# Kernel optimization log

Hardware: AMD Instinct MI355X
Metric: run time of the kernel (lower is better)

Reference implementation:

```python
import jax, jax.numpy as jnp
import numpy as np

TOKENS = 512
IN_F = 8192
OUT_F = 8192
RANK = 64
NNZ = 8192
QMAX = 127.0  # int8 symmetric


def setup_inputs() -> dict:
    key = jax.random.key(0)
    ks = jax.random.split(key, 12)
    x = jax.random.normal(ks[0], (TOKENS, IN_F), dtype=jnp.float32)
    quantized_weight = jax.random.randint(ks[1], (OUT_F, IN_F), -128, 128, dtype=jnp.int32)
    weight_scale = jax.random.uniform(ks[2], (OUT_F,), minval=0.005, maxval=0.02, dtype=jnp.float32)
    smooth_scales = jax.random.uniform(ks[3], (IN_F,), minval=0.5, maxval=2.0, dtype=jnp.float32)
    act_scale = jnp.array([0.05], dtype=jnp.float32)
    outlier_rows = jax.random.randint(ks[4], (NNZ,), 0, OUT_F, dtype=jnp.int32)
    outlier_cols = jax.random.randint(ks[5], (NNZ,), 0, IN_F, dtype=jnp.int32)
    outlier_vals = jax.random.normal(ks[6], (NNZ,), dtype=jnp.float32) * 0.1
    svd_U = jax.random.normal(ks[7], (OUT_F, RANK), dtype=jnp.float32) * 0.02
    svd_S = jax.random.uniform(ks[8], (RANK,), minval=0.1, maxval=1.0, dtype=jnp.float32)
    svd_V = jax.random.normal(ks[9], (IN_F, RANK), dtype=jnp.float32) * 0.02
    bias = jax.random.normal(ks[10], (OUT_F,), dtype=jnp.float32) * 0.01
    return {"x": x, "quantized_weight": quantized_weight, "weight_scale": weight_scale,
            "smooth_scales": smooth_scales, "act_scale": act_scale,
            "outlier_rows": outlier_rows, "outlier_cols": outlier_cols,
            "outlier_vals": outlier_vals, "svd_U": svd_U, "svd_S": svd_S,
            "svd_V": svd_V, "bias": bias}


def reference(x, quantized_weight, weight_scale, smooth_scales, act_scale,
              outlier_rows, outlier_cols, outlier_vals, svd_U, svd_S, svd_V, bias):
    # SmoothQuant: migrate activation outliers into the weight scales
    x_s = x / smooth_scales  # [T, in]
    # per-tensor symmetric int8 activation fake-quant
    a = act_scale[0]
    x_q = jnp.clip(jnp.round(x_s / a), -QMAX - 1.0, QMAX)
    x_dq = x_q * a  # [T, in]
    # dequantize weight: per-output-channel scale, plus sparse outlier correction
    W = quantized_weight.astype(jnp.float32) * weight_scale[:, None]  # [out, in]
    W = W.at[outlier_rows, outlier_cols].add(outlier_vals)
    # dense quantized matmul
    y = x_dq @ W.T  # [T, out]
    # low-rank SVD residual: x @ (U S V^T)^T = ((x @ V) * S) @ U^T
    y = y + ((x_dq @ svd_V) * svd_S) @ svd_U.T
    return y + bias
```

## Files before the change

### kernel.cpp

```cpp
#include <hip/hip_runtime.h>
#include <hip/hip_bf16.h>

#define TOKENS 512
#define IN_F 8192
#define OUT_F 8192
#define RANK 64
#define NNZ 8192

#define KSPLIT 4
#define KRANGE (IN_F / KSPLIT)
#define BM 512
#define BN 64
#define BK 64
#define NT (KRANGE / BK)

typedef __attribute__((ext_vector_type(8))) short short8;
typedef __attribute__((ext_vector_type(4))) float f32x4;
typedef __attribute__((ext_vector_type(4))) int int4v;

__device__ __forceinline__ unsigned short f2bf(float f) {
  unsigned int u = __builtin_bit_cast(unsigned int, f);
  u += 0x7FFFu + ((u >> 16) & 1u);
  return (unsigned short)(u >> 16);
}
__device__ __forceinline__ float bf2f(unsigned short b) {
  unsigned int u = ((unsigned int)b) << 16;
  return __builtin_bit_cast(float, u);
}

__device__ __forceinline__ void gload_lds16(const void* g, void* l) {
  __builtin_amdgcn_global_load_lds(
      (const __attribute__((address_space(1))) unsigned int*)(g),
      (__attribute__((address_space(3))) unsigned int*)(l), 16, 0, 0);
}

#define WAIT_VM(n) asm volatile("s_waitcnt vmcnt(" #n ")" ::: "memory")
#define WAIT_LGKM0 asm volatile("s_waitcnt lgkmcnt(0)" ::: "memory")

__global__ __launch_bounds__(256) void k_quant(const float* __restrict__ x,
                                               const float* __restrict__ smooth,
                                               const float* __restrict__ act,
                                               unsigned short* __restrict__ Abf,
                                               unsigned char* __restrict__ Aq) {
  int idx = blockIdx.x * 256 + threadIdx.x;
  int base = idx * 4;
  int col = base & (IN_F - 1);
  float a = act[0];
  float4 xx = *(const float4*)(x + base);
  float4 ss = *(const float4*)(smooth + col);
  float q0 = fminf(fmaxf(rintf((xx.x / ss.x) / a), -128.f), 127.f);
  float q1 = fminf(fmaxf(rintf((xx.y / ss.y) / a), -128.f), 127.f);
  float q2 = fminf(fmaxf(rintf((xx.z / ss.z) / a), -128.f), 127.f);
  float q3 = fminf(fmaxf(rintf((xx.w / ss.w) / a), -128.f), 127.f);
  ushort4 o;
  o.x = f2bf(q0); o.y = f2bf(q1); o.z = f2bf(q2); o.w = f2bf(q3);
  *(ushort4*)(Abf + base) = o;
  int i0 = (int)q0, i1 = (int)q1, i2 = (int)q2, i3 = (int)q3;
  unsigned int p = (i0 & 0xFF) | ((i1 & 0xFF) << 8) | ((i2 & 0xFF) << 16) |
                   ((unsigned)(i3 & 0xFF) << 24);
  *(unsigned int*)(Aq + base) = p;
}

__global__ __launch_bounds__(256) void k_lr1(const unsigned short* __restrict__ Abf,
                                             const float* __restrict__ V,
                                             const float* __restrict__ S,
                                             const float* __restrict__ act,
                                             float* __restrict__ t) {
  int bid = blockIdx.x;
  int mb = (bid & 3) * 128;
  int kb0 = (bid >> 2) * 512;
  int tid = threadIdx.x, w = tid >> 6, l = tid & 63;
  int lr = l & 15, lg = l >> 4;
  f32x4 acc[2][4] = {};
  for (int ks = 0; ks < 16; ++ks) {
    int kb = kb0 + ks * 32;
    short8 af[2];
#pragma unroll
    for (int fi = 0; fi < 2; ++fi) {
      int row = mb + w * 32 + fi * 16 + lr;
      af[fi] = *(const short8*)(Abf + (size_t)row * IN_F + kb + lg * 8);
    }
    short8 bfr[4];
#pragma unroll
    for (int fj = 0; fj < 4; ++fj) {
      int rk = fj * 16 + lr;
      short8 bv;
#pragma unroll
      for (int j = 0; j < 8; ++j)
        bv[j] = (short)f2bf(V[(size_t)(kb + lg * 8 + j) * RANK + rk]);
      bfr[fj] = bv;
    }
#pragma unroll
    for (int fi = 0; fi < 2; ++fi)
#pragma unroll
      for (int fj = 0; fj < 4; ++fj)
        acc[fi][fj] = __builtin_amdgcn_mfma_f32_16x16x32_bf16(af[fi], bfr[fj], acc[fi][fj], 0, 0, 0);
  }
  float a = act[0];
#pragma unroll
  for (int fi = 0; fi < 2; ++fi)
#pragma unroll
    for (int fj = 0; fj < 4; ++fj) {
      int rk = fj * 16 + lr;
      float sc = a * S[rk];
#pragma unroll
      for (int r = 0; r < 4; ++r) {
        int tok = mb + w * 32 + fi * 16 + lg * 4 + r;
        atomicAdd(t + tok * RANK + rk, acc[fi][fj][r] * sc);
      }
    }
}

__global__ __launch_bounds__(256) void k_lr2(const float* __restrict__ t,
                                             const float* __restrict__ U,
                                             const float* __restrict__ bias,
                                             float* __restrict__ out) {
  int bid = blockIdx.x;
  int mb = (bid & 3) * 128;
  int nb = (bid >> 2) * 128;
  int tid = threadIdx.x, w = tid >> 6, l = tid & 63;
  int lr = l & 15, lg = l >> 4;
  int wm = w >> 1, wn = w & 1;
  f32x4 acc[4][4] = {};
#pragma unroll
  for (int kk = 0; kk < 2; ++kk) {
    short8 af[4], bfr[4];
#pragma unroll
    for (int fi = 0; fi < 4; ++fi) {
      int row = mb + wm * 64 + fi * 16 + lr;
      const float4* tp = (const float4*)(t + (size_t)row * RANK + kk * 32 + lg * 8);
      float4 t0 = tp[0], t1 = tp[1];
      af[fi][0] = f2bf(t0.x); af[fi][1] = f2bf(t0.y);
      af[fi][2] = f2bf(t0.z); af[fi][3] = f2bf(t0.w);
      af[fi][4] = f2bf(t1.x); af[fi][5] = f2bf(t1.y);
      af[fi][6] = f2bf(t1.z); af[fi][7] = f2bf(t1.w);
    }
#pragma unroll
    for (int fj = 0; fj < 4; ++fj) {
      int row = nb + wn * 64 + fj * 16 + lr;
      const float4* up = (const float4*)(U + (size_t)row * RANK + kk * 32 + lg * 8);
      float4 u0 = up[0], u1 = up[1];
      bfr[fj][0] = f2bf(u0.x); bfr[fj][1] = f2bf(u0.y);
      bfr[fj][2] = f2bf(u0.z); bfr[fj][3] = f2bf(u0.w);
      bfr[fj][4] = f2bf(u1.x); bfr[fj][5] = f2bf(u1.y);
      bfr[fj][6] = f2bf(u1.z); bfr[fj][7] = f2bf(u1.w);
    }
#pragma unroll
    for (int fi = 0; fi < 4; ++fi)
#pragma unroll
      for (int fj = 0; fj < 4; ++fj)
        acc[fi][fj] = __builtin_amdgcn_mfma_f32_16x16x32_bf16(af[fi], bfr[fj], acc[fi][fj], 0, 0, 0);
  }
#pragma unroll
  for (int fj = 0; fj < 4; ++fj) {
    int o = nb + wn * 64 + fj * 16 + lr;
    float b = bias[o];
#pragma unroll
    for (int fi = 0; fi < 4; ++fi)
#pragma unroll
      for (int r = 0; r < 4; ++r) {
        int tok = mb + wm * 64 + fi * 16 + lg * 4 + r;
        out[(size_t)tok * OUT_F + o] = b + acc[fi][fj][r];
      }
  }
}

__global__ __launch_bounds__(256) void k_outlier_merge(
    const unsigned short* __restrict__ Abf, const int* __restrict__ rows,
    const int* __restrict__ cols, const float* __restrict__ vals,
    const float* __restrict__ act, const float* __restrict__ wscale,
    const int* __restrict__ part, float* __restrict__ out) {
  __shared__ float accr[OUT_F];
  int tk = blockIdx.x;
  for (int i = threadIdx.x; i < OUT_F; i += 256) accr[i] = 0.f;
  __syncthreads();
  float a = act[0];
  for (int i = threadIdx.x; i < NNZ; i += 256) {
    int r = rows[i], c = cols[i];
    float v = vals[i];
    float xq = bf2f(Abf[(size_t)tk * IN_F + c]);
    atomicAdd(accr + r, a * xq * v);
  }
  __syncthreads();
  float* orow = out + (size_t)tk * OUT_F;
  const int* p0 = part + (size_t)tk * OUT_F;
  const int* p1 = p0 + (size_t)TOKENS * OUT_F;
  const int* p2 = p1 + (size_t)TOKENS * OUT_F;
  const int* p3 = p2 + (size_t)TOKENS * OUT_F;
  for (int i = threadIdx.x * 4; i < OUT_F; i += 1024) {
    int4v s0 = *(const int4v*)(p0 + i);
    int4v s1 = *(const int4v*)(p1 + i);
    int4v s2 = *(const int4v*)(p2 + i);
    int4v s3 = *(const int4v*)(p3 + i);
    float4 ws = *(const float4*)(wscale + i);
    float4 ov = *(const float4*)(orow + i);
    ov.x += accr[i + 0] + (float)(s0[0] + s1[0] + s2[0] + s3[0]) * a * ws.x;
    ov.y += accr[i + 1] + (float)(s0[1] + s1[1] + s2[1] + s3[1]) * a * ws.y;
    ov.z += accr[i + 2] + (float)(s0[2] + s1[2] + s2[2] + s3[2]) * a * ws.z;
    ov.w += accr[i + 3] + (float)(s0[3] + s1[3] + s2[3] + s3[3]) * a * ws.w;
    *(float4*)(orow + i) = ov;
  }
}

__global__ __launch_bounds__(512, 4) void k_gemm(const unsigned char* __restrict__ Aq,
                                                 const int* __restrict__ W,
                                                 int* __restrict__ part) {
  __shared__ __align__(16) unsigned char As[2][BM * BK];
  __shared__ __align__(16) unsigned char Bs[2][BN * BK];

  int d = blockIdx.x;
  int wg = (d & 7) * 64 + (d >> 3);
  int ks = wg >> 7;
  int nb = wg & 127;
  int kb0 = ks * KRANGE;

  int tid = threadIdx.x, w = tid >> 6, l = tid & 63;
  int lr = l & 15, lg = l >> 4;
  int wm = w >> 1, wn = w & 1;

  int4v acc[8][2] = {};
  int4v wa[2], wb[2];

  const int rB = tid >> 3;
  const int kcB = (tid & 7) * 8;

  auto LOAD_W = [&](int4v (&wr)[2], int kb) {
    const int* wp = W + (size_t)(nb * BN + rB) * IN_F + kb + kcB;
    wr[0] = *(const int4v*)wp;
    wr[1] = *(const int4v*)(wp + 4);
  };
  auto STAGE_A = [&](int buf, int kb) {
#pragma unroll
    for (int i = 0; i < 4; ++i) {
      int ubase = i * 512 + w * 64;
      int ell = ubase + l;
      int r = ell >> 2, up = ell & 3;
      int u = up ^ ((r >> 1) & 3);
      gload_lds16(Aq + (size_t)r * IN_F + kb + u * 16, &As[buf][(size_t)ubase * 16]);
    }
  };
  auto WRITE_B = [&](int buf, const int4v (&wr)[2]) {
    unsigned int w0 = 0, w1 = 0;
#pragma unroll
    for (int j = 0; j < 4; ++j) w0 |= ((unsigned)(wr[0][j] & 0xFF)) << (8 * j);
#pragma unroll
    for (int j = 0; j < 4; ++j) w1 |= ((unsigned)(wr[1][j] & 0xFF)) << (8 * j);
    int u = kcB >> 4, sub = (kcB >> 3) & 1;
    int us = u ^ ((rB >> 1) & 3);
    uint2 val; val.x = w0; val.y = w1;
    *(uint2*)(&Bs[buf][(size_t)rB * BK + us * 16 + sub * 8]) = val;
  };
  auto LDFA = [&](int buf, int row) -> int4v {
    int u = lg ^ ((row >> 1) & 3);
    return *(const int4v*)(&As[buf][(size_t)row * BK + u * 16]);
  };
  auto LDFB = [&](int buf, int row) -> int4v {
    int u = lg ^ ((row >> 1) & 3);
    return *(const int4v*)(&Bs[buf][(size_t)row * BK + u * 16]);
  };
  auto COMPUTE = [&](int buf) {
    __builtin_amdgcn_s_setprio(1);
    int4v b0 = LDFB(buf, wn * 32 + lr);
    int4v b1 = LDFB(buf, wn * 32 + 16 + lr);
#pragma unroll
    for (int fi = 0; fi < 8; ++fi) {
      int4v af = LDFA(buf, wm * 128 + fi * 16 + lr);
      acc[fi][0] = __builtin_amdgcn_mfma_i32_16x16x64_i8(af, b0, acc[fi][0], 0, 0, 0);
      acc[fi][1] = __builtin_amdgcn_mfma_i32_16x16x64_i8(af, b1, acc[fi][1], 0, 0, 0);
    }
    __builtin_amdgcn_s_setprio(0);
  };

  LOAD_W(wa, kb0);
  STAGE_A(0, kb0);
  WAIT_VM(4);
  WRITE_B(0, wa);
  LOAD_W(wa, kb0 + BK);
  WAIT_VM(2);
  WAIT_LGKM0;
  __builtin_amdgcn_s_barrier();

#define ITER(kt, CUR, wcur, wnxt)                                   \
  {                                                                 \
    STAGE_A(CUR ^ 1, kb0 + (((kt) + 1) & (NT - 1)) * BK);           \
    LOAD_W(wnxt, kb0 + (((kt) + 2) & (NT - 1)) * BK);               \
    COMPUTE(CUR);                                                   \
    WAIT_VM(6);                                                     \
    WRITE_B(CUR ^ 1, wcur);                                         \
    WAIT_VM(2);                                                     \
    WAIT_LGKM0;                                                     \
    __builtin_amdgcn_s_barrier();                                   \
  }

  for (int kt = 0; kt < NT; kt += 2) {
    ITER(kt, 0, wa, wb);
    ITER(kt + 1, 1, wb, wa);
  }
#undef ITER

  int* pp = part + (size_t)ks * TOKENS * OUT_F;
#pragma unroll
  for (int fj = 0; fj < 2; ++fj) {
    int o = nb * BN + wn * 32 + fj * 16 + lr;
#pragma unroll
    for (int fi = 0; fi < 8; ++fi)
#pragma unroll
      for (int rr = 0; rr < 4; ++rr) {
        int tok = wm * 128 + fi * 16 + lg * 4 + rr;
        pp[(size_t)tok * OUT_F + o] = acc[fi][fj][rr];
      }
  }
}

extern "C" void kernel_launch(void* const* d_in, const int* in_sizes, int n_in,
                              void* d_out, int out_size, void* d_ws, size_t ws_size,
                              hipStream_t stream) {
  const float* x = (const float*)d_in[0];
  const int* W = (const int*)d_in[1];
  const float* wscale = (const float*)d_in[2];
  const float* smooth = (const float*)d_in[3];
  const float* act = (const float*)d_in[4];
  const int* orow = (const int*)d_in[5];
  const int* ocol = (const int*)d_in[6];
  const float* oval = (const float*)d_in[7];
  const float* U = (const float*)d_in[8];
  const float* S = (const float*)d_in[9];
  const float* V = (const float*)d_in[10];
  const float* bias = (const float*)d_in[11];
  float* out = (float*)d_out;

  unsigned short* Abf = (unsigned short*)d_ws;
  unsigned char* Aq = (unsigned char*)d_ws + (size_t)TOKENS * IN_F * 2;
  float* t = (float*)((char*)d_ws + (size_t)TOKENS * IN_F * 3);
  int* part = (int*)((char*)d_ws + (size_t)TOKENS * IN_F * 3 + (size_t)TOKENS * RANK * 4);

  hipMemsetAsync(t, 0, TOKENS * RANK * sizeof(float), stream);
  k_quant<<<(TOKENS * IN_F / 4) / 256, 256, 0, stream>>>(x, smooth, act, Abf, Aq);
  k_gemm<<<512, 512, 0, stream>>>(Aq, W, part);
  k_lr1<<<64, 256, 0, stream>>>(Abf, V, S, act, t);
  k_lr2<<<256, 256, 0, stream>>>(t, U, bias, out);
  k_outlier_merge<<<TOKENS, 256, 0, stream>>>(Abf, orow, ocol, oval, act,
                                              wscale, part, out);
}
```

Measured before the change: 191.1 us.

## Widen GEMM N-tile to 128 with 1024-thread blocks and triple-buffered LDS

The int8 GEMM now uses BN=128 tiles and 1024-thread workgroups, so half as many blocks launch (256) and each warp holds a 4x4 fragment grid instead of 8x2. LDS staging moves from double to triple buffering, with A prefetched two k-steps ahead, plus sched_barrier fences around the workgroup barriers. The aim is to halve redundant A-tile traffic per output column, raise MFMA work per LDS fragment load, and hide global-load latency better. The cost is more LDS per block and fewer blocks per CU, and 256 blocks may leave some of the device's compute units without work.

```diff
diff --git a/kernel.cpp b/kernel.cpp
--- a/kernel.cpp
+++ b/kernel.cpp
@@ -10,7 +10,7 @@
 #define KSPLIT 4
 #define KRANGE (IN_F / KSPLIT)
 #define BM 512
-#define BN 64
+#define BN 128
 #define BK 64
 #define NT (KRANGE / BK)
 
@@ -36,6 +36,7 @@
 
 #define WAIT_VM(n) asm volatile("s_waitcnt vmcnt(" #n ")" ::: "memory")
 #define WAIT_LGKM0 asm volatile("s_waitcnt lgkmcnt(0)" ::: "memory")
+#define SCHED0 __builtin_amdgcn_sched_barrier(0)
 
 __global__ __launch_bounds__(256) void k_quant(const float* __restrict__ x,
                                                const float* __restrict__ smooth,
@@ -202,53 +203,55 @@
   }
 }
 
-__global__ __launch_bounds__(512, 4) void k_gemm(const unsigned char* __restrict__ Aq,
-                                                 const int* __restrict__ W,
-                                                 int* __restrict__ part) {
-  __shared__ __align__(16) unsigned char As[2][BM * BK];
-  __shared__ __align__(16) unsigned char Bs[2][BN * BK];
+__global__ __launch_bounds__(1024, 4) void k_gemm(const unsigned char* __restrict__ Aq,
+                                                  const int* __restrict__ W,
+                                                  int* __restrict__ part) {
+  __shared__ __align__(16) unsigned char As[3][BM * BK];
+  __shared__ __align__(16) unsigned char Bs[3][BN * BK];
 
   int d = blockIdx.x;
-  int wg = (d & 7) * 64 + (d >> 3);
-  int ks = wg >> 7;
-  int nb = wg & 127;
+  int wg = (d & 7) * 32 + (d >> 3);
+  int ks = wg >> 6;
+  int nb = wg & 63;
   int kb0 = ks * KRANGE;
 
   int tid = threadIdx.x, w = tid >> 6, l = tid & 63;
   int lr = l & 15, lg = l >> 4;
   int wm = w >> 1, wn = w & 1;
 
-  int4v acc[8][2] = {};
+  int4v acc[4][4] = {};
   int4v wa[2], wb[2];
 
-  const int rB = tid >> 3;
-  const int kcB = (tid & 7) * 8;
-
-  auto LOAD_W = [&](int4v (&wr)[2], int kb) {
-    const int* wp = W + (size_t)(nb * BN + rB) * IN_F + kb + kcB;
+  const int rW = tid >> 3;
+  const int kcW = (tid & 7) * 8;
+  const int uW = (kcW >> 4) ^ ((rW >> 1) & 3);
+  const int offW = kcW & 15;
+
+  auto LOAD_W = [&](int4v (&wr)[2], int kt) {
+    const int* wp = W + (size_t)(nb * BN + rW) * IN_F + kb0 +
+                    (kt & (NT - 1)) * BK + kcW;
     wr[0] = *(const int4v*)wp;
     wr[1] = *(const int4v*)(wp + 4);
   };
-  auto STAGE_A = [&](int buf, int kb) {
-#pragma unroll
-    for (int i = 0; i < 4; ++i) {
-      int ubase = i * 512 + w * 64;
-      int ell = ubase + l;
-      int r = ell >> 2, up = ell & 3;
+  auto STAGE_A = [&](int buf, int kt) {
+    int kb = kb0 + (kt & (NT - 1)) * BK;
+#pragma unroll
+    for (int i = 0; i < 2; ++i) {
+      int lidx = i * 1024 + w * 64;
+      int U = lidx + l;
+      int r = U >> 2, up = U & 3;
       int u = up ^ ((r >> 1) & 3);
-      gload_lds16(Aq + (size_t)r * IN_F + kb + u * 16, &As[buf][(size_t)ubase * 16]);
-    }
-  };
-  auto WRITE_B = [&](int buf, const int4v (&wr)[2]) {
+      gload_lds16(Aq + (size_t)r * IN_F + kb + u * 16, &As[buf][(size_t)lidx * 16]);
+    }
+  };
+  auto DSWRITE_B = [&](int buf, const int4v (&wr)[2]) {
     unsigned int w0 = 0, w1 = 0;
 #pragma unroll
     for (int j = 0; j < 4; ++j) w0 |= ((unsigned)(wr[0][j] & 0xFF)) << (8 * j);
 #pragma unroll
     for (int j = 0; j < 4; ++j) w1 |= ((unsigned)(wr[1][j] & 0xFF)) << (8 * j);
-    int u = kcB >> 4, sub = (kcB >> 3) & 1;
-    int us = u ^ ((rB >> 1) & 3);
     uint2 val; val.x = w0; val.y = w1;
-    *(uint2*)(&Bs[buf][(size_t)rB * BK + us * 16 + sub * 8]) = val;
+    *(uint2*)(&Bs[buf][(size_t)rW * BK + uW * 16 + offW]) = val;
   };
   auto LDFA = [&](int buf, int row) -> int4v {
     int u = lg ^ ((row >> 1) & 3);
@@ -259,54 +262,67 @@
     return *(const int4v*)(&Bs[buf][(size_t)row * BK + u * 16]);
   };
   auto COMPUTE = [&](int buf) {
+    int4v b0 = LDFB(buf, wn * 64 + 0 * 16 + lr);
+    int4v b1 = LDFB(buf, wn * 64 + 1 * 16 + lr);
+    int4v b2 = LDFB(buf, wn * 64 + 2 * 16 + lr);
+    int4v b3 = LDFB(buf, wn * 64 + 3 * 16 + lr);
     __builtin_amdgcn_s_setprio(1);
-    int4v b0 = LDFB(buf, wn * 32 + lr);
-    int4v b1 = LDFB(buf, wn * 32 + 16 + lr);
-#pragma unroll
-    for (int fi = 0; fi < 8; ++fi) {
-      int4v af = LDFA(buf, wm * 128 + fi * 16 + lr);
+#pragma unroll
+    for (int fi = 0; fi < 4; ++fi) {
+      int4v af = LDFA(buf, wm * 64 + fi * 16 + lr);
       acc[fi][0] = __builtin_amdgcn_mfma_i32_16x16x64_i8(af, b0, acc[fi][0], 0, 0, 0);
       acc[fi][1] = __builtin_amdgcn_mfma_i32_16x16x64_i8(af, b1, acc[fi][1], 0, 0, 0);
+      acc[fi][2] = __builtin_amdgcn_mfma_i32_16x16x64_i8(af, b2, acc[fi][2], 0, 0, 0);
+      acc[fi][3] = __builtin_amdgcn_mfma_i32_16x16x64_i8(af, b3, acc[fi][3], 0, 0, 0);
     }
     __builtin_amdgcn_s_setprio(0);
   };
 
-  LOAD_W(wa, kb0);
-  STAGE_A(0, kb0);
+  STAGE_A(0, 0);
+  LOAD_W(wa, 0);
+  STAGE_A(1, 1);
+  LOAD_W(wb, 1);
   WAIT_VM(4);
-  WRITE_B(0, wa);
-  LOAD_W(wa, kb0 + BK);
-  WAIT_VM(2);
+  DSWRITE_B(0, wa);
   WAIT_LGKM0;
+  SCHED0;
   __builtin_amdgcn_s_barrier();
-
-#define ITER(kt, CUR, wcur, wnxt)                                   \
-  {                                                                 \
-    STAGE_A(CUR ^ 1, kb0 + (((kt) + 1) & (NT - 1)) * BK);           \
-    LOAD_W(wnxt, kb0 + (((kt) + 2) & (NT - 1)) * BK);               \
-    COMPUTE(CUR);                                                   \
-    WAIT_VM(6);                                                     \
-    WRITE_B(CUR ^ 1, wcur);                                         \
-    WAIT_VM(2);                                                     \
-    WAIT_LGKM0;                                                     \
-    __builtin_amdgcn_s_barrier();                                   \
-  }
-
+  SCHED0;
+
+  int c = 0;
   for (int kt = 0; kt < NT; kt += 2) {
-    ITER(kt, 0, wa, wb);
-    ITER(kt + 1, 1, wb, wa);
-  }
-#undef ITER
+    int c1 = c + 1 == 3 ? 0 : c + 1;
+    int c2 = c1 + 1 == 3 ? 0 : c1 + 1;
+    STAGE_A(c2, kt + 2);
+    LOAD_W(wa, kt + 2);
+    COMPUTE(c);
+    WAIT_VM(4);
+    DSWRITE_B(c1, wb);
+    WAIT_LGKM0;
+    SCHED0;
+    __builtin_amdgcn_s_barrier();
+    SCHED0;
+    STAGE_A(c, kt + 3);
+    LOAD_W(wb, kt + 3);
+    COMPUTE(c1);
+    WAIT_VM(4);
+    DSWRITE_B(c2, wa);
+    WAIT_LGKM0;
+    SCHED0;
+    __builtin_amdgcn_s_barrier();
+    SCHED0;
+    c = c2;
+  }
 
   int* pp = part + (size_t)ks * TOKENS * OUT_F;
 #pragma unroll
-  for (int fj = 0; fj < 2; ++fj) {
-    int o = nb * BN + wn * 32 + fj * 16 + lr;
-#pragma unroll
-    for (int fi = 0; fi < 8; ++fi)
+  for (int fj = 0; fj < 4; ++fj) {
+    int o = nb * BN + wn * 64 + fj * 16 + lr;
+#pragma unroll
+    for (int fi = 0; fi < 4; ++fi)
 #pragma unroll
       for (int rr = 0; rr < 4; ++rr) {
-        int tok = wm * 128 + fi * 16 + lg * 4 + rr;
+        int tok = wm * 64 + fi * 16 + lg * 4 + rr;
         pp[(size_t)tok * OUT_F + o] = acc[fi][fj][rr];
       }
   }
@@ -332,11 +348,12 @@
   unsigned short* Abf = (unsigned short*)d_ws;
   unsigned char* Aq = (unsigned char*)d_ws + (size_t)TOKENS * IN_F * 2;
   float* t = (float*)((char*)d_ws + (size_t)TOKENS * IN_F * 3);
-  int* part = (int*)((char*)d_ws + (size_t)TOKENS * IN_F * 3 + (size_t)TOKENS * RANK * 4);
+  int* part = (int*)((char*)d_ws + (size_t)TOKENS * IN_F * 3 +
+                     (size_t)TOKENS * RANK * 4);
 
   hipMemsetAsync(t, 0, TOKENS * RANK * sizeof(float), stream);
   k_quant<<<(TOKENS * IN_F / 4) / 256, 256, 0, stream>>>(x, smooth, act, Abf, Aq);
-  k_gemm<<<512, 512, 0, stream>>>(Aq, W, part);
+  k_gemm<<<256, 1024, 0, stream>>>(Aq, W, part);
   k_lr1<<<64, 256, 0, stream>>>(Abf, V, S, act, t);
   k_lr2<<<256, 256, 0, stream>>>(t, U, bias, out);
   k_outlier_merge<<<TOKENS, 256, 0, stream>>>(Abf, orow, ocol, oval, act,
```

New measurement: 185.6 us, median of 2. -2.9%, faster.

## Replace low-rank atomics with split partials and tighten GEMM pipeline scheduling

Applied to the files above, without the earlier changes.

The first low-rank kernel now writes per-K-split partial results to separate buffers instead of using atomicAdd, and the second low-rank kernel sums the 16 partials when it loads them. This removes the memset and the atomic contention. The int8 GEMM loop moves the B LDS write after a single vmcnt wait, sets priority only after the B fragment loads, and adds sched_barriers around the workgroup barrier to control instruction ordering. In exchange, workspace use grows and lr2 reads 16 times more data for t.

```diff
diff --git a/kernel.cpp b/kernel.cpp
--- a/kernel.cpp
+++ b/kernel.cpp
@@ -13,6 +13,7 @@
 #define BN 64
 #define BK 64
 #define NT (KRANGE / BK)
+#define LRSPLIT 16
 
 typedef __attribute__((ext_vector_type(8))) short short8;
 typedef __attribute__((ext_vector_type(4))) float f32x4;
@@ -36,6 +37,7 @@
 
 #define WAIT_VM(n) asm volatile("s_waitcnt vmcnt(" #n ")" ::: "memory")
 #define WAIT_LGKM0 asm volatile("s_waitcnt lgkmcnt(0)" ::: "memory")
+#define SCHED0 __builtin_amdgcn_sched_barrier(0)
 
 __global__ __launch_bounds__(256) void k_quant(const float* __restrict__ x,
                                                const float* __restrict__ smooth,
@@ -68,7 +70,8 @@
                                              float* __restrict__ t) {
   int bid = blockIdx.x;
   int mb = (bid & 3) * 128;
-  int kb0 = (bid >> 2) * 512;
+  int ksp = bid >> 2;
+  int kb0 = ksp * 512;
   int tid = threadIdx.x, w = tid >> 6, l = tid & 63;
   int lr = l & 15, lg = l >> 4;
   f32x4 acc[2][4] = {};
@@ -97,6 +100,7 @@
         acc[fi][fj] = __builtin_amdgcn_mfma_f32_16x16x32_bf16(af[fi], bfr[fj], acc[fi][fj], 0, 0, 0);
   }
   float a = act[0];
+  float* tk = t + (size_t)ksp * TOKENS * RANK;
 #pragma unroll
   for (int fi = 0; fi < 2; ++fi)
 #pragma unroll
@@ -106,7 +110,7 @@
 #pragma unroll
       for (int r = 0; r < 4; ++r) {
         int tok = mb + w * 32 + fi * 16 + lg * 4 + r;
-        atomicAdd(t + tok * RANK + rk, acc[fi][fj][r] * sc);
+        tk[(size_t)tok * RANK + rk] = acc[fi][fj][r] * sc;
       }
     }
 }
@@ -128,8 +132,14 @@
 #pragma unroll
     for (int fi = 0; fi < 4; ++fi) {
       int row = mb + wm * 64 + fi * 16 + lr;
-      const float4* tp = (const float4*)(t + (size_t)row * RANK + kk * 32 + lg * 8);
-      float4 t0 = tp[0], t1 = tp[1];
+      size_t off = (size_t)row * RANK + kk * 32 + lg * 8;
+      float4 t0 = {0, 0, 0, 0}, t1 = {0, 0, 0, 0};
+      for (int s = 0; s < LRSPLIT; ++s) {
+        const float4* tp = (const float4*)(t + (size_t)s * TOKENS * RANK + off);
+        float4 u0 = tp[0], u1 = tp[1];
+        t0.x += u0.x; t0.y += u0.y; t0.z += u0.z; t0.w += u0.w;
+        t1.x += u1.x; t1.y += u1.y; t1.z += u1.z; t1.w += u1.w;
+      }
       af[fi][0] = f2bf(t0.x); af[fi][1] = f2bf(t0.y);
       af[fi][2] = f2bf(t0.z); af[fi][3] = f2bf(t0.w);
       af[fi][4] = f2bf(t1.x); af[fi][5] = f2bf(t1.y);
@@ -221,34 +231,36 @@
   int4v acc[8][2] = {};
   int4v wa[2], wb[2];
 
-  const int rB = tid >> 3;
-  const int kcB = (tid & 7) * 8;
-
-  auto LOAD_W = [&](int4v (&wr)[2], int kb) {
-    const int* wp = W + (size_t)(nb * BN + rB) * IN_F + kb + kcB;
+  const int rW = tid >> 3;
+  const int kcW = (tid & 7) * 8;
+  const int uW = (kcW >> 4) ^ ((rW >> 1) & 3);
+  const int offW = kcW & 15;
+
+  auto LOAD_W = [&](int4v (&wr)[2], int kt) {
+    const int* wp = W + (size_t)(nb * BN + rW) * IN_F + kb0 +
+                    (kt & (NT - 1)) * BK + kcW;
     wr[0] = *(const int4v*)wp;
     wr[1] = *(const int4v*)(wp + 4);
   };
-  auto STAGE_A = [&](int buf, int kb) {
+  auto STAGE_A = [&](int buf, int kt) {
+    int kb = kb0 + (kt & (NT - 1)) * BK;
 #pragma unroll
     for (int i = 0; i < 4; ++i) {
-      int ubase = i * 512 + w * 64;
-      int ell = ubase + l;
-      int r = ell >> 2, up = ell & 3;
+      int lidx = i * 512 + w * 64;
+      int U = lidx + l;
+      int r = U >> 2, up = U & 3;
       int u = up ^ ((r >> 1) & 3);
-      gload_lds16(Aq + (size_t)r * IN_F + kb + u * 16, &As[buf][(size_t)ubase * 16]);
-    }
-  };
-  auto WRITE_B = [&](int buf, const int4v (&wr)[2]) {
+      gload_lds16(Aq + (size_t)r * IN_F + kb + u * 16, &As[buf][(size_t)lidx * 16]);
+    }
+  };
+  auto DSWRITE_B = [&](int buf, const int4v (&wr)[2]) {
     unsigned int w0 = 0, w1 = 0;
 #pragma unroll
     for (int j = 0; j < 4; ++j) w0 |= ((unsigned)(wr[0][j] & 0xFF)) << (8 * j);
 #pragma unroll
     for (int j = 0; j < 4; ++j) w1 |= ((unsigned)(wr[1][j] & 0xFF)) << (8 * j);
-    int u = kcB >> 4, sub = (kcB >> 3) & 1;
-    int us = u ^ ((rB >> 1) & 3);
     uint2 val; val.x = w0; val.y = w1;
-    *(uint2*)(&Bs[buf][(size_t)rB * BK + us * 16 + sub * 8]) = val;
+    *(uint2*)(&Bs[buf][(size_t)rW * BK + uW * 16 + offW]) = val;
   };
   auto LDFA = [&](int buf, int row) -> int4v {
     int u = lg ^ ((row >> 1) & 3);
@@ -259,9 +271,9 @@
     return *(const int4v*)(&Bs[buf][(size_t)row * BK + u * 16]);
   };
   auto COMPUTE = [&](int buf) {
-    __builtin_amdgcn_s_setprio(1);
     int4v b0 = LDFB(buf, wn * 32 + lr);
     int4v b1 = LDFB(buf, wn * 32 + 16 + lr);
+    __builtin_amdgcn_s_setprio(1);
 #pragma unroll
     for (int fi = 0; fi < 8; ++fi) {
       int4v af = LDFA(buf, wm * 128 + fi * 16 + lr);
@@ -271,25 +283,28 @@
     __builtin_amdgcn_s_setprio(0);
   };
 
-  LOAD_W(wa, kb0);
-  STAGE_A(0, kb0);
+  LOAD_W(wa, 0);
+  STAGE_A(0, 0);
   WAIT_VM(4);
-  WRITE_B(0, wa);
-  LOAD_W(wa, kb0 + BK);
+  DSWRITE_B(0, wa);
+  LOAD_W(wa, 1);
   WAIT_VM(2);
   WAIT_LGKM0;
+  SCHED0;
   __builtin_amdgcn_s_barrier();
+  SCHED0;
 
 #define ITER(kt, CUR, wcur, wnxt)                                   \
   {                                                                 \
-    STAGE_A(CUR ^ 1, kb0 + (((kt) + 1) & (NT - 1)) * BK);           \
-    LOAD_W(wnxt, kb0 + (((kt) + 2) & (NT - 1)) * BK);               \
+    STAGE_A(CUR ^ 1, (kt) + 1);                                     \
+    LOAD_W(wnxt, (kt) + 2);                                         \
     COMPUTE(CUR);                                                   \
-    WAIT_VM(6);                                                     \
-    WRITE_B(CUR ^ 1, wcur);                                         \
     WAIT_VM(2);                                                     \
+    DSWRITE_B(CUR ^ 1, wcur);                                       \
     WAIT_LGKM0;                                                     \
+    SCHED0;                                                         \
     __builtin_amdgcn_s_barrier();                                   \
+    SCHED0;                                                         \
   }
 
   for (int kt = 0; kt < NT; kt += 2) {
@@ -332,9 +347,9 @@
   unsigned short* Abf = (unsigned short*)d_ws;
   unsigned char* Aq = (unsigned char*)d_ws + (size_t)TOKENS * IN_F * 2;
   float* t = (float*)((char*)d_ws + (size_t)TOKENS * IN_F * 3);
-  int* part = (int*)((char*)d_ws + (size_t)TOKENS * IN_F * 3 + (size_t)TOKENS * RANK * 4);
-
-  hipMemsetAsync(t, 0, TOKENS * RANK * sizeof(float), stream);
+  int* part = (int*)((char*)d_ws + (size_t)TOKENS * IN_F * 3 +
+                     (size_t)LRSPLIT * TOKENS * RANK * 4);
+
   k_quant<<<(TOKENS * IN_F / 4) / 256, 256, 0, stream>>>(x, smooth, act, Abf, Aq);
   k_gemm<<<512, 512, 0, stream>>>(Aq, W, part);
   k_lr1<<<64, 256, 0, stream>>>(Abf, V, S, act, t);
```

Measured after the change: 208.9 us. +9.3%, slower.
